# Kernel tuning notes

Measured on AMD Instinct MI355X. Metric: run time of the kernel, lower is better.

The kernel has to match this reference:

```python
import jax, jax.numpy as jnp
import numpy as np

N_NODES = 100000


def gcn_conv(x, src, dst, norm, W, b, n_nodes):
    # x: [N, Din]; src/dst: [E'] (with self-loops); norm: [E']
    h = x @ W  # [N, Dout] dense transform first (PyG GCNConv order)
    msgs = h[src] * norm[:, None]  # gather + degree scaling, [E', Dout]
    out = jax.ops.segment_sum(msgs, dst, num_segments=n_nodes)  # scatter-add
    return out + b


def setup_inputs() -> dict:
    key = jax.random.key(0)
    k_x, k_e, k_w1, k_w2 = jax.random.split(key, 4)
    input_dim, hidden_dim = 256, 128
    n_edges = 1600000
    x = jax.random.normal(k_x, (N_NODES, input_dim), dtype=jnp.float32)
    edge_index = jax.random.randint(k_e, (2, n_edges), 0, N_NODES, dtype=jnp.int64)
    # Glorot-style init for conv weights, zeros bias (PyG defaults)
    s1 = (6.0 / (input_dim + hidden_dim)) ** 0.5
    s2 = (6.0 / (hidden_dim + hidden_dim)) ** 0.5
    W1 = jax.random.uniform(k_w1, (input_dim, hidden_dim), jnp.float32, -s1, s1)
    W2 = jax.random.uniform(k_w2, (hidden_dim, hidden_dim), jnp.float32, -s2, s2)
    b1 = jnp.zeros((hidden_dim,), jnp.float32)
    b2 = jnp.zeros((hidden_dim,), jnp.float32)
    return {"x": x, "edge_index": edge_index, "W1": W1, "b1": b1, "W2": W2, "b2": b2}


def reference(x, edge_index, W1, b1, W2, b2):
    n = x.shape[0]
    loops = jnp.arange(n, dtype=edge_index.dtype)
    src = jnp.concatenate([edge_index[0], loops])  # add self-loops
    dst = jnp.concatenate([edge_index[1], loops])
    # symmetric normalization deg^-1/2 (in-degree including self-loops)
    deg = jax.ops.segment_sum(jnp.ones_like(dst, dtype=x.dtype), dst, num_segments=n)
    dinv = jax.lax.rsqrt(deg)
    norm = dinv[src] * dinv[dst]
    # layer 1: GCNConv -> ReLU (dropout is identity in eval mode)
    h = jax.nn.relu(gcn_conv(x, src, dst, norm, W1, b1, n))
    # layer 2
    h = jax.nn.relu(gcn_conv(h, src, dst, norm, W2, b2, n))
    return h
```

## Files before the change

kernel.cpp:

```cpp
#include <hip/hip_runtime.h>
#include <hip/hip_bf16.h>


#define DIN 256
#define DH 128
#define BKT_SHIFT 9
#define BKT_SZ 512
#define NBKT_MAX 256
#define CAP 10240

typedef __attribute__((ext_vector_type(8))) short short8;
typedef __attribute__((ext_vector_type(4))) float f32x4;
typedef __attribute__((ext_vector_type(2))) unsigned int uint2e;

__device__ __forceinline__ unsigned short f2bf(float f) {
    union { float f; unsigned int i; } c;
    c.f = f;
    unsigned int r = c.i + 0x7FFFu + ((c.i >> 16) & 1u);
    return (unsigned short)(r >> 16);
}
__device__ __forceinline__ float bf_lo(unsigned int u) {
    union { unsigned int i; float f; } c;
    c.i = u << 16;
    return c.f;
}
__device__ __forceinline__ float bf_hi(unsigned int u) {
    union { unsigned int i; float f; } c;
    c.i = u & 0xFFFF0000u;
    return c.f;
}

__global__ __launch_bounds__(256) void prep_k(const int* __restrict__ src,
                                              const int* __restrict__ dst,
                                              int* __restrict__ bcnt,
                                              int* __restrict__ tmp, int e, int n,
                                              int NBB,
                                              const float* __restrict__ W1,
                                              const float* __restrict__ W2,
                                              unsigned short* __restrict__ Wt1,
                                              unsigned short* __restrict__ Wt2) {
    int bx = blockIdx.x;
    int t = threadIdx.x;
    if (bx >= NBB) {
        int i = (bx - NBB) * 256 + t;
        if (i < 256 * 128) {
            int k = i >> 7, nn = i & 127;
            Wt1[(size_t)nn * 256 + k] = f2bf(W1[i]);
        } else if (i < 256 * 128 + 128 * 128) {
            int j = i - 256 * 128;
            int k = j >> 7, nn = j & 127;
            Wt2[(size_t)nn * 128 + k] = f2bf(W2[j]);
        }
        return;
    }
    __shared__ int hist[NBKT_MAX];
    __shared__ int rstart[NBKT_MAX];
    int nbkt = (n + BKT_SZ - 1) >> BKT_SHIFT;
    int chunk = (e + NBB - 1) / NBB;
    int beg = bx * chunk, end = min(e, beg + chunk);

    hist[t] = 0;
    __syncthreads();
    for (int i = beg + t; i < end; i += 256) atomicAdd(&hist[dst[i] >> BKT_SHIFT], 1);
    __syncthreads();
    int h = hist[t];
    if (t < nbkt && h > 0) rstart[t] = atomicAdd(&bcnt[t], h);
    __syncthreads();
    hist[t] = 0;
    __syncthreads();
    for (int i = beg + t; i < end; i += 256) {
        int d = dst[i];
        int b = d >> BKT_SHIFT;
        int o = atomicAdd(&hist[b], 1);
        tmp[(size_t)b * CAP + rstart[b] + o] = src[i] | ((d & (BKT_SZ - 1)) << 20);
    }
}

__global__ void scan196_k(const int* __restrict__ bcnt, int* __restrict__ base,
                          int* __restrict__ rowptr, int nbkt, int n) {
    __shared__ int s[256];
    int t = threadIdx.x;
    s[t] = (t < nbkt) ? bcnt[t] : 0;
    __syncthreads();
    for (int off = 1; off < 256; off <<= 1) {
        int x = (t >= off) ? s[t - off] : 0;
        __syncthreads();
        s[t] += x;
        __syncthreads();
    }
    base[t] = (t == 0) ? 0 : s[t - 1];
    if (t == nbkt - 1) {
        base[nbkt] = s[t];
        rowptr[n] = s[t];
    }
}

__global__ __launch_bounds__(1024) void scatter2_k(const int* __restrict__ tmp,
                                                   const int* __restrict__ bcnt,
                                                   const int* __restrict__ base,
                                                   float* __restrict__ dinv,
                                                   int* __restrict__ rowptr,
                                                   int* __restrict__ einfo, int n) {
    __shared__ int hist[BKT_SZ];
    __shared__ int scn[BKT_SZ];
    __shared__ int cur[BKT_SZ];
    int b = blockIdx.x;
    int t = threadIdx.x;
    int lo = b << BKT_SHIFT;
    int nn = min(n - lo, BKT_SZ);
    int cnt = bcnt[b];
    int bas = base[b];
    const int* rec = tmp + (size_t)b * CAP;
    if (t < BKT_SZ) hist[t] = 0;
    __syncthreads();
    for (int i = t; i < cnt; i += 1024) atomicAdd(&hist[(rec[i] >> 20) & (BKT_SZ - 1)], 1);
    __syncthreads();
    if (t < BKT_SZ) scn[t] = hist[t];
    __syncthreads();
    for (int off = 1; off < BKT_SZ; off <<= 1) {
        int x = 0;
        if (t < BKT_SZ && t >= off) x = scn[t - off];
        __syncthreads();
        if (t < BKT_SZ) scn[t] += x;
        __syncthreads();
    }
    if (t < nn) {
        int excl = bas + scn[t] - hist[t];
        dinv[lo + t] = 1.0f / sqrtf((float)(hist[t] + 1));
        rowptr[lo + t] = excl;
        cur[t] = excl;
    }
    __syncthreads();
    for (int i = t; i < cnt; i += 1024) {
        int r = rec[i];
        int dlow = (r >> 20) & (BKT_SZ - 1);
        int pos = atomicAdd(&cur[dlow], 1);
        einfo[pos] = r & 0xFFFFF;
    }
}

template <bool A_BF16>
__global__ __launch_bounds__(256) void gemm_mfma(const void* __restrict__ Av,
                                                 const unsigned short* __restrict__ Wt,
                                                 const float* __restrict__ dinv,
                                                 unsigned short* __restrict__ Hb,
                                                 int M, int K) {
    __shared__ unsigned short Bt[16384];
    const int t = threadIdx.x;
    const int w = t >> 6;
    const int lane = t & 63;
    const int l15 = lane & 15;
    const int quad = lane >> 4;
    const int row0 = blockIdx.x * 128 + w * 32;

    const float* Af = (const float*)Av;
    const unsigned short* Ab = (const unsigned short*)Av;

    f32x4 acc[2][8];
#pragma unroll
    for (int rt = 0; rt < 2; ++rt)
#pragma unroll
        for (int ct = 0; ct < 8; ++ct)
#pragma unroll
            for (int j = 0; j < 4; ++j) acc[rt][ct][j] = 0.0f;

    for (int kc = 0; kc < K; kc += 128) {
        if (kc) __syncthreads();
#pragma unroll
        for (int i = 0; i < 8; ++i) {
            int fg = w * 8 + i;
            int ks = fg >> 3, ct = fg & 7;
            int nn = ct * 16 + l15;
            int gk = ks * 32 + quad * 8;
            *(short8*)&Bt[fg * 512 + lane * 8] =
                *(const short8*)(Wt + (size_t)nn * K + kc + gk);
        }
        __syncthreads();
#pragma unroll
        for (int ks = 0; ks < 4; ++ks) {
            int kk = ks * 32 + quad * 8;
            short8 af[2];
#pragma unroll
            for (int rt = 0; rt < 2; ++rt) {
                int row = row0 + rt * 16 + l15;
                if (row < M) {
                    if (A_BF16) {
                        af[rt] = *(const short8*)(Ab + (size_t)row * K + kc + kk);
                    } else {
                        const float* p = Af + (size_t)row * K + kc + kk;
                        float4 x0 = *(const float4*)p;
                        float4 x1 = *(const float4*)(p + 4);
                        af[rt][0] = (short)f2bf(x0.x);
                        af[rt][1] = (short)f2bf(x0.y);
                        af[rt][2] = (short)f2bf(x0.z);
                        af[rt][3] = (short)f2bf(x0.w);
                        af[rt][4] = (short)f2bf(x1.x);
                        af[rt][5] = (short)f2bf(x1.y);
                        af[rt][6] = (short)f2bf(x1.z);
                        af[rt][7] = (short)f2bf(x1.w);
                    }
                } else {
#pragma unroll
                    for (int j = 0; j < 8; ++j) af[rt][j] = 0;
                }
            }
#pragma unroll
            for (int ct = 0; ct < 8; ++ct) {
                short8 bfr = *(const short8*)&Bt[(ks * 8 + ct) * 512 + lane * 8];
                acc[0][ct] = __builtin_amdgcn_mfma_f32_16x16x32_bf16(af[0], bfr, acc[0][ct], 0, 0, 0);
                acc[1][ct] = __builtin_amdgcn_mfma_f32_16x16x32_bf16(af[1], bfr, acc[1][ct], 0, 0, 0);
            }
        }
    }
#pragma unroll
    for (int rt = 0; rt < 2; ++rt)
#pragma unroll
        for (int r = 0; r < 4; ++r) {
            int row = row0 + rt * 16 + quad * 4 + r;
            if (row < M) {
                float dv = dinv[row];
                unsigned short* o = Hb + (size_t)row * 128 + l15;
#pragma unroll
                for (int ct = 0; ct < 8; ++ct) o[ct * 16] = f2bf(dv * acc[rt][ct][r]);
            }
        }
}

template <bool OUT_BF16>
__global__ __launch_bounds__(256) void agg_k(const unsigned short* __restrict__ Hb,
                                             const int* __restrict__ rowptr,
                                             const int* __restrict__ einfo,
                                             const float* __restrict__ dinv,
                                             const float* __restrict__ bias,
                                             void* __restrict__ out, int n) {
    int v = blockIdx.x * 4 + (threadIdx.x >> 6);
    int lane = threadIdx.x & 63;
    if (v >= n) return;
    int l = lane & 31, half = lane >> 5;
    const uint2* __restrict__ H = (const uint2*)Hb;
    float a0 = 0.f, a1 = 0.f, a2 = 0.f, a3 = 0.f;
    if (half == 0) {
        uint2 hv = H[(size_t)v * 32 + l];
        a0 = bf_lo(hv.x); a1 = bf_hi(hv.x);
        a2 = bf_lo(hv.y); a3 = bf_hi(hv.y);
    }
    int end = rowptr[v + 1];
    int i = rowptr[v] + half;
    for (; i + 6 < end; i += 8) {
        int s0 = __builtin_nontemporal_load(&einfo[i]);
        int s1 = __builtin_nontemporal_load(&einfo[i + 2]);
        int s2 = __builtin_nontemporal_load(&einfo[i + 4]);
        int s3 = __builtin_nontemporal_load(&einfo[i + 6]);
        uint2 v0 = H[(size_t)s0 * 32 + l];
        uint2 v1 = H[(size_t)s1 * 32 + l];
        uint2 v2 = H[(size_t)s2 * 32 + l];
        uint2 v3 = H[(size_t)s3 * 32 + l];
        a0 += bf_lo(v0.x); a1 += bf_hi(v0.x); a2 += bf_lo(v0.y); a3 += bf_hi(v0.y);
        a0 += bf_lo(v1.x); a1 += bf_hi(v1.x); a2 += bf_lo(v1.y); a3 += bf_hi(v1.y);
        a0 += bf_lo(v2.x); a1 += bf_hi(v2.x); a2 += bf_lo(v2.y); a3 += bf_hi(v2.y);
        a0 += bf_lo(v3.x); a1 += bf_hi(v3.x); a2 += bf_lo(v3.y); a3 += bf_hi(v3.y);
    }
    for (; i < end; i += 2) {
        int s = __builtin_nontemporal_load(&einfo[i]);
        uint2 vv = H[(size_t)s * 32 + l];
        a0 += bf_lo(vv.x); a1 += bf_hi(vv.x); a2 += bf_lo(vv.y); a3 += bf_hi(vv.y);
    }
    a0 += __shfl_xor(a0, 32);
    a1 += __shfl_xor(a1, 32);
    a2 += __shfl_xor(a2, 32);
    a3 += __shfl_xor(a3, 32);
    if (half == 0) {
        float dv = dinv[v];
        float4 bb = ((const float4*)bias)[l];
        float o0 = fmaxf(fmaf(dv, a0, bb.x), 0.f);
        float o1 = fmaxf(fmaf(dv, a1, bb.y), 0.f);
        float o2 = fmaxf(fmaf(dv, a2, bb.z), 0.f);
        float o3 = fmaxf(fmaf(dv, a3, bb.w), 0.f);
        if (OUT_BF16) {
            uint2e p;
            p.x = (unsigned int)f2bf(o0) | ((unsigned int)f2bf(o1) << 16);
            p.y = (unsigned int)f2bf(o2) | ((unsigned int)f2bf(o3) << 16);
            __builtin_nontemporal_store(p, (uint2e*)out + (size_t)v * 32 + l);
        } else {
            f32x4 o = {o0, o1, o2, o3};
            __builtin_nontemporal_store(o, (f32x4*)out + (size_t)v * 32 + l);
        }
    }
}

static inline size_t align_up(size_t x, size_t a) { return (x + a - 1) & ~(a - 1); }

extern "C" void kernel_launch(void* const* d_in, const int* in_sizes, int n_in,
                              void* d_out, int out_size, void* d_ws, size_t ws_size,
                              hipStream_t stream) {
    const float* x  = (const float*)d_in[0];
    const int*   ei = (const int*)d_in[1];
    const float* W1 = (const float*)d_in[2];
    const float* b1 = (const float*)d_in[3];
    const float* W2 = (const float*)d_in[4];
    const float* b2 = (const float*)d_in[5];

    const int N = in_sizes[0] / DIN;
    const int E = in_sizes[1] / 2;
    const int* src = ei;
    const int* dst = ei + E;
    const int NBKT = (N + BKT_SZ - 1) >> BKT_SHIFT;

    char* base_p = (char*)d_ws;
    size_t off = 0;
    int* bcnt = (int*)(base_p + off);       off = align_up(off + 256 * 4, 256);
    int* bbase = (int*)(base_p + off);      off = align_up(off + 257 * 4, 256);
    int* rowptr = (int*)(base_p + off);     off = align_up(off + (size_t)(N + 1) * 4, 256);
    float* dinv = (float*)(base_p + off);   off = align_up(off + (size_t)N * 4, 256);
    int* tmp = (int*)(base_p + off);        off = align_up(off + (size_t)NBKT * CAP * 4, 256);
    int* einfo = (int*)(base_p + off);      off = align_up(off + (size_t)E * 4, 256);
    unsigned short* Wt1 = (unsigned short*)(base_p + off); off = align_up(off + (size_t)128 * 256 * 2, 256);
    unsigned short* Wt2 = (unsigned short*)(base_p + off); off = align_up(off + (size_t)128 * 128 * 2, 256);
    unsigned short* hb  = (unsigned short*)(base_p + off); off = align_up(off + (size_t)N * 128 * 2, 256);
    unsigned short* a1b = (unsigned short*)(base_p + off); off = align_up(off + (size_t)N * 128 * 2, 256);

    float* out = (float*)d_out;

    const int NBB = 512;
    const int WTB = (256 * 128 + 128 * 128 + 255) / 256;

    hipMemsetAsync(bcnt, 0, 256 * sizeof(int), stream);
    prep_k<<<NBB + WTB, 256, 0, stream>>>(src, dst, bcnt, tmp, E, N, NBB, W1, W2, Wt1, Wt2);
    scan196_k<<<1, 256, 0, stream>>>(bcnt, bbase, rowptr, NBKT, N);
    scatter2_k<<<NBKT, 1024, 0, stream>>>(tmp, bcnt, bbase, dinv, rowptr, einfo, N);

    const int GB = (N + 127) / 128;
    gemm_mfma<false><<<GB, 256, 0, stream>>>(x, Wt1, dinv, hb, N, DIN);
    agg_k<true><<<(N + 3) / 4, 256, 0, stream>>>(hb, rowptr, einfo, dinv, b1, a1b, N);
    gemm_mfma<true><<<GB, 256, 0, stream>>>(a1b, Wt2, dinv, hb, N, DH);
    agg_k<false><<<(N + 3) / 4, 256, 0, stream>>>(hb, rowptr, einfo, dinv, b2, out, N);
}
```

Before: 429.3 us.

## Fuse edge bucketing with layer-1 GEMM and fold scan into scatter

Layer 1's GEMM no longer depends on dinv. It now runs in the same launch as the edge-bucketing blocks, and the source-side degree scaling moves into the first aggregation as a per-edge dinv gather. The single-block bucket scan is folded into scatter2_k, where each block redoes the 256-entry scan. The memset is replaced by a zeroing block in the weight-convert kernel. Together this cuts launches and serial dependencies at the cost of an extra random dinv load per edge in layer-1 aggregation.

```diff
diff --git a/kernel.cpp b/kernel.cpp
--- a/kernel.cpp
+++ b/kernel.cpp
@@ -30,128 +30,41 @@
     return c.f;
 }
 
-__global__ __launch_bounds__(256) void prep_k(const int* __restrict__ src,
-                                              const int* __restrict__ dst,
-                                              int* __restrict__ bcnt,
-                                              int* __restrict__ tmp, int e, int n,
-                                              int NBB,
-                                              const float* __restrict__ W1,
-                                              const float* __restrict__ W2,
-                                              unsigned short* __restrict__ Wt1,
-                                              unsigned short* __restrict__ Wt2) {
+__global__ __launch_bounds__(256) void cvt_zero_k(const float* __restrict__ W1,
+                                                  const float* __restrict__ W2,
+                                                  unsigned short* __restrict__ Wt1,
+                                                  unsigned short* __restrict__ Wt2,
+                                                  int* __restrict__ bcnt, int WTB) {
     int bx = blockIdx.x;
     int t = threadIdx.x;
-    if (bx >= NBB) {
-        int i = (bx - NBB) * 256 + t;
-        if (i < 256 * 128) {
-            int k = i >> 7, nn = i & 127;
-            Wt1[(size_t)nn * 256 + k] = f2bf(W1[i]);
-        } else if (i < 256 * 128 + 128 * 128) {
-            int j = i - 256 * 128;
-            int k = j >> 7, nn = j & 127;
-            Wt2[(size_t)nn * 128 + k] = f2bf(W2[j]);
-        }
+    if (bx >= WTB) {
+        bcnt[t] = 0;
         return;
     }
-    __shared__ int hist[NBKT_MAX];
-    __shared__ int rstart[NBKT_MAX];
-    int nbkt = (n + BKT_SZ - 1) >> BKT_SHIFT;
-    int chunk = (e + NBB - 1) / NBB;
-    int beg = bx * chunk, end = min(e, beg + chunk);
-
-    hist[t] = 0;
-    __syncthreads();
-    for (int i = beg + t; i < end; i += 256) atomicAdd(&hist[dst[i] >> BKT_SHIFT], 1);
-    __syncthreads();
-    int h = hist[t];
-    if (t < nbkt && h > 0) rstart[t] = atomicAdd(&bcnt[t], h);
-    __syncthreads();
-    hist[t] = 0;
-    __syncthreads();
-    for (int i = beg + t; i < end; i += 256) {
-        int d = dst[i];
-        int b = d >> BKT_SHIFT;
-        int o = atomicAdd(&hist[b], 1);
-        tmp[(size_t)b * CAP + rstart[b] + o] = src[i] | ((d & (BKT_SZ - 1)) << 20);
-    }
-}
-
-__global__ void scan196_k(const int* __restrict__ bcnt, int* __restrict__ base,
-                          int* __restrict__ rowptr, int nbkt, int n) {
-    __shared__ int s[256];
-    int t = threadIdx.x;
-    s[t] = (t < nbkt) ? bcnt[t] : 0;
-    __syncthreads();
-    for (int off = 1; off < 256; off <<= 1) {
-        int x = (t >= off) ? s[t - off] : 0;
-        __syncthreads();
-        s[t] += x;
-        __syncthreads();
-    }
-    base[t] = (t == 0) ? 0 : s[t - 1];
-    if (t == nbkt - 1) {
-        base[nbkt] = s[t];
-        rowptr[n] = s[t];
-    }
-}
-
-__global__ __launch_bounds__(1024) void scatter2_k(const int* __restrict__ tmp,
-                                                   const int* __restrict__ bcnt,
-                                                   const int* __restrict__ base,
-                                                   float* __restrict__ dinv,
-                                                   int* __restrict__ rowptr,
-                                                   int* __restrict__ einfo, int n) {
-    __shared__ int hist[BKT_SZ];
-    __shared__ int scn[BKT_SZ];
-    __shared__ int cur[BKT_SZ];
-    int b = blockIdx.x;
-    int t = threadIdx.x;
-    int lo = b << BKT_SHIFT;
-    int nn = min(n - lo, BKT_SZ);
-    int cnt = bcnt[b];
-    int bas = base[b];
-    const int* rec = tmp + (size_t)b * CAP;
-    if (t < BKT_SZ) hist[t] = 0;
-    __syncthreads();
-    for (int i = t; i < cnt; i += 1024) atomicAdd(&hist[(rec[i] >> 20) & (BKT_SZ - 1)], 1);
-    __syncthreads();
-    if (t < BKT_SZ) scn[t] = hist[t];
-    __syncthreads();
-    for (int off = 1; off < BKT_SZ; off <<= 1) {
-        int x = 0;
-        if (t < BKT_SZ && t >= off) x = scn[t - off];
-        __syncthreads();
-        if (t < BKT_SZ) scn[t] += x;
-        __syncthreads();
-    }
-    if (t < nn) {
-        int excl = bas + scn[t] - hist[t];
-        dinv[lo + t] = 1.0f / sqrtf((float)(hist[t] + 1));
-        rowptr[lo + t] = excl;
-        cur[t] = excl;
-    }
-    __syncthreads();
-    for (int i = t; i < cnt; i += 1024) {
-        int r = rec[i];
-        int dlow = (r >> 20) & (BKT_SZ - 1);
-        int pos = atomicAdd(&cur[dlow], 1);
-        einfo[pos] = r & 0xFFFFF;
-    }
-}
-
-template <bool A_BF16>
-__global__ __launch_bounds__(256) void gemm_mfma(const void* __restrict__ Av,
-                                                 const unsigned short* __restrict__ Wt,
-                                                 const float* __restrict__ dinv,
-                                                 unsigned short* __restrict__ Hb,
-                                                 int M, int K) {
-    __shared__ unsigned short Bt[16384];
+    int i = bx * 256 + t;
+    if (i < 256 * 128) {
+        int k = i >> 7, nn = i & 127;
+        Wt1[(size_t)nn * 256 + k] = f2bf(W1[i]);
+    } else {
+        int j = i - 256 * 128;
+        int k = j >> 7, nn = j & 127;
+        Wt2[(size_t)nn * 128 + k] = f2bf(W2[j]);
+    }
+}
+
+template <bool A_BF16, bool SCALE>
+__device__ __forceinline__ void gemm_body(unsigned short* Bt, int gb,
+                                          const void* __restrict__ Av,
+                                          const unsigned short* __restrict__ Wt,
+                                          const float* __restrict__ dinv,
+                                          unsigned short* __restrict__ Hb,
+                                          int M, int K) {
     const int t = threadIdx.x;
     const int w = t >> 6;
     const int lane = t & 63;
     const int l15 = lane & 15;
     const int quad = lane >> 4;
-    const int row0 = blockIdx.x * 128 + w * 32;
+    const int row0 = gb * 128 + w * 32;
 
     const float* Af = (const float*)Av;
     const unsigned short* Ab = (const unsigned short*)Av;
@@ -218,15 +131,121 @@
         for (int r = 0; r < 4; ++r) {
             int row = row0 + rt * 16 + quad * 4 + r;
             if (row < M) {
-                float dv = dinv[row];
+                float dv = SCALE ? dinv[row] : 1.0f;
                 unsigned short* o = Hb + (size_t)row * 128 + l15;
 #pragma unroll
-                for (int ct = 0; ct < 8; ++ct) o[ct * 16] = f2bf(dv * acc[rt][ct][r]);
+                for (int ct = 0; ct < 8; ++ct)
+                    o[ct * 16] = f2bf(SCALE ? dv * acc[rt][ct][r] : acc[rt][ct][r]);
             }
         }
 }
 
-template <bool OUT_BF16>
+struct SmemFused {
+    union {
+        unsigned short Bt[16384];
+        struct {
+            int hist[NBKT_MAX];
+            int rstart[NBKT_MAX];
+        } bk;
+    };
+};
+
+__global__ __launch_bounds__(256) void fused1_k(const int* __restrict__ src,
+                                                const int* __restrict__ dst,
+                                                int* __restrict__ bcnt,
+                                                int* __restrict__ tmp, int e, int n,
+                                                int NBB,
+                                                const float* __restrict__ x,
+                                                const unsigned short* __restrict__ Wt1,
+                                                unsigned short* __restrict__ hb, int M) {
+    __shared__ SmemFused sm;
+    int bx = blockIdx.x;
+    int t = threadIdx.x;
+    if (bx < NBB) {
+        int* hist = sm.bk.hist;
+        int* rstart = sm.bk.rstart;
+        int chunk = (e + NBB - 1) / NBB;
+        int beg = bx * chunk, end = min(e, beg + chunk);
+
+        hist[t] = 0;
+        __syncthreads();
+        for (int i = beg + t; i < end; i += 256) atomicAdd(&hist[dst[i] >> BKT_SHIFT], 1);
+        __syncthreads();
+        int nbkt = (n + BKT_SZ - 1) >> BKT_SHIFT;
+        int h = hist[t];
+        if (t < nbkt && h > 0) rstart[t] = atomicAdd(&bcnt[t], h);
+        __syncthreads();
+        hist[t] = 0;
+        __syncthreads();
+        for (int i = beg + t; i < end; i += 256) {
+            int d = dst[i];
+            int b = d >> BKT_SHIFT;
+            int o = atomicAdd(&hist[b], 1);
+            tmp[(size_t)b * CAP + rstart[b] + o] = src[i] | ((d & (BKT_SZ - 1)) << 20);
+        }
+        return;
+    }
+    gemm_body<false, false>(sm.Bt, bx - NBB, x, Wt1, nullptr, hb, M, DIN);
+}
+
+__global__ __launch_bounds__(1024) void scatter2_k(const int* __restrict__ tmp,
+                                                   const int* __restrict__ bcnt,
+                                                   float* __restrict__ dinv,
+                                                   int* __restrict__ rowptr,
+                                                   int* __restrict__ einfo, int n,
+                                                   int nbkt) {
+    __shared__ int hist[BKT_SZ];
+    __shared__ int scn[BKT_SZ];
+    __shared__ int cur[BKT_SZ];
+    int b = blockIdx.x;
+    int t = threadIdx.x;
+    int lo = b << BKT_SHIFT;
+    int nn = min(n - lo, BKT_SZ);
+    int cnt = bcnt[b];
+    const int* rec = tmp + (size_t)b * CAP;
+
+    if (t < 256) scn[t] = (t < nbkt) ? bcnt[t] : 0;
+    __syncthreads();
+    for (int off = 1; off < 256; off <<= 1) {
+        int v = 0;
+        if (t < 256 && t >= off) v = scn[t - off];
+        __syncthreads();
+        if (t < 256) scn[t] += v;
+        __syncthreads();
+    }
+    int bas = scn[b] - cnt;
+    if (b == nbkt - 1 && t == 0) rowptr[n] = scn[nbkt - 1];
+    __syncthreads();
+
+    if (t < BKT_SZ) hist[t] = 0;
+    __syncthreads();
+    for (int i = t; i < cnt; i += 1024) atomicAdd(&hist[(rec[i] >> 20) & (BKT_SZ - 1)], 1);
+    __syncthreads();
+    if (t < BKT_SZ) scn[t] = hist[t];
+    __syncthreads();
+    for (int off = 1; off < BKT_SZ; off <<= 1) {
+        int v = 0;
+        if (t < BKT_SZ && t >= off) v = scn[t - off];
+        __syncthreads();
+        if (t < BKT_SZ) scn[t] += v;
+        __syncthreads();
+    }
+    if (t < nn) {
+        int excl = bas + scn[t] - hist[t];
+        dinv[lo + t] = 1.0f / sqrtf((float)(hist[t] + 1));
+        rowptr[lo + t] = excl;
+        cur[t] = excl;
+    }
+    __syncthreads();
+    for (int i = t; i < cnt; i += 1024) {
+        int r = rec[i];
+        int dlow = (r >> 20) & (BKT_SZ - 1);
+        int pos = atomicAdd(&cur[dlow], 1);
+        einfo[pos] = r & 0xFFFFF;
+    }
+}
+
+template <bool SCALE_SRC, bool OUT_BF16>
 __global__ __launch_bounds__(256) void agg_k(const unsigned short* __restrict__ Hb,
                                              const int* __restrict__ rowptr,
                                              const int* __restrict__ einfo,
@@ -238,11 +257,17 @@
     if (v >= n) return;
     int l = lane & 31, half = lane >> 5;
     const uint2* __restrict__ H = (const uint2*)Hb;
+    float dv = dinv[v];
     float a0 = 0.f, a1 = 0.f, a2 = 0.f, a3 = 0.f;
     if (half == 0) {
         uint2 hv = H[(size_t)v * 32 + l];
-        a0 = bf_lo(hv.x); a1 = bf_hi(hv.x);
-        a2 = bf_lo(hv.y); a3 = bf_hi(hv.y);
+        if (SCALE_SRC) {
+            a0 = dv * bf_lo(hv.x); a1 = dv * bf_hi(hv.x);
+            a2 = dv * bf_lo(hv.y); a3 = dv * bf_hi(hv.y);
+        } else {
+            a0 = bf_lo(hv.x); a1 = bf_hi(hv.x);
+            a2 = bf_lo(hv.y); a3 = bf_hi(hv.y);
+        }
     }
     int end = rowptr[v + 1];
     int i = rowptr[v] + half;
@@ -251,26 +276,44 @@
         int s1 = __builtin_nontemporal_load(&einfo[i + 2]);
         int s2 = __builtin_nontemporal_load(&einfo[i + 4]);
         int s3 = __builtin_nontemporal_load(&einfo[i + 6]);
+        float d0 = 1.f, d1 = 1.f, d2 = 1.f, d3 = 1.f;
+        if (SCALE_SRC) { d0 = dinv[s0]; d1 = dinv[s1]; d2 = dinv[s2]; d3 = dinv[s3]; }
         uint2 v0 = H[(size_t)s0 * 32 + l];
         uint2 v1 = H[(size_t)s1 * 32 + l];
         uint2 v2 = H[(size_t)s2 * 32 + l];
         uint2 v3 = H[(size_t)s3 * 32 + l];
-        a0 += bf_lo(v0.x); a1 += bf_hi(v0.x); a2 += bf_lo(v0.y); a3 += bf_hi(v0.y);
-        a0 += bf_lo(v1.x); a1 += bf_hi(v1.x); a2 += bf_lo(v1.y); a3 += bf_hi(v1.y);
-        a0 += bf_lo(v2.x); a1 += bf_hi(v2.x); a2 += bf_lo(v2.y); a3 += bf_hi(v2.y);
-        a0 += bf_lo(v3.x); a1 += bf_hi(v3.x); a2 += bf_lo(v3.y); a3 += bf_hi(v3.y);
+        if (SCALE_SRC) {
+            a0 = fmaf(d0, bf_lo(v0.x), a0); a1 = fmaf(d0, bf_hi(v0.x), a1);
+            a2 = fmaf(d0, bf_lo(v0.y), a2); a3 = fmaf(d0, bf_hi(v0.y), a3);
+            a0 = fmaf(d1, bf_lo(v1.x), a0); a1 = fmaf(d1, bf_hi(v1.x), a1);
+            a2 = fmaf(d1, bf_lo(v1.y), a2); a3 = fmaf(d1, bf_hi(v1.y), a3);
+            a0 = fmaf(d2, bf_lo(v2.x), a0); a1 = fmaf(d2, bf_hi(v2.x), a1);
+            a2 = fmaf(d2, bf_lo(v2.y), a2); a3 = fmaf(d2, bf_hi(v2.y), a3);
+            a0 = fmaf(d3, bf_lo(v3.x), a0); a1 = fmaf(d3, bf_hi(v3.x), a1);
+            a2 = fmaf(d3, bf_lo(v3.y), a2); a3 = fmaf(d3, bf_hi(v3.y), a3);
+        } else {
+            a0 += bf_lo(v0.x); a1 += bf_hi(v0.x); a2 += bf_lo(v0.y); a3 += bf_hi(v0.y);
+            a0 += bf_lo(v1.x); a1 += bf_hi(v1.x); a2 += bf_lo(v1.y); a3 += bf_hi(v1.y);
+            a0 += bf_lo(v2.x); a1 += bf_hi(v2.x); a2 += bf_lo(v2.y); a3 += bf_hi(v2.y);
+            a0 += bf_lo(v3.x); a1 += bf_hi(v3.x); a2 += bf_lo(v3.y); a3 += bf_hi(v3.y);
+        }
     }
     for (; i < end; i += 2) {
         int s = __builtin_nontemporal_load(&einfo[i]);
+        float ds = SCALE_SRC ? dinv[s] : 1.f;
         uint2 vv = H[(size_t)s * 32 + l];
-        a0 += bf_lo(vv.x); a1 += bf_hi(vv.x); a2 += bf_lo(vv.y); a3 += bf_hi(vv.y);
+        if (SCALE_SRC) {
+            a0 = fmaf(ds, bf_lo(vv.x), a0); a1 = fmaf(ds, bf_hi(vv.x), a1);
+            a2 = fmaf(ds, bf_lo(vv.y), a2); a3 = fmaf(ds, bf_hi(vv.y), a3);
+        } else {
+            a0 += bf_lo(vv.x); a1 += bf_hi(vv.x); a2 += bf_lo(vv.y); a3 += bf_hi(vv.y);
+        }
     }
     a0 += __shfl_xor(a0, 32);
     a1 += __shfl_xor(a1, 32);
     a2 += __shfl_xor(a2, 32);
     a3 += __shfl_xor(a3, 32);
     if (half == 0) {
-        float dv = dinv[v];
         float4 bb = ((const float4*)bias)[l];
         float o0 = fmaxf(fmaf(dv, a0, bb.x), 0.f);
         float o1 = fmaxf(fmaf(dv, a1, bb.y), 0.f);
@@ -288,6 +331,15 @@
     }
 }
 
+__global__ __launch_bounds__(256) void gemm2_k(const unsigned short* __restrict__ A,
+                                               const unsigned short* __restrict__ Wt,
+                                               const float* __restrict__ dinv,
+                                               unsigned short* __restrict__ Hb,
+                                               int M, int K) {
+    __shared__ unsigned short Bt[16384];
+    gemm_body<true, true>(Bt, blockIdx.x, A, Wt, dinv, Hb, M, K);
+}
+
 static inline size_t align_up(size_t x, size_t a) { return (x + a - 1) & ~(a - 1); }
 
 extern "C" void kernel_launch(void* const* d_in, const int* in_sizes, int n_in,
@@ -309,7 +361,6 @@
     char* base_p = (char*)d_ws;
     size_t off = 0;
     int* bcnt = (int*)(base_p + off);       off = align_up(off + 256 * 4, 256);
-    int* bbase = (int*)(base_p + off);      off = align_up(off + 257 * 4, 256);
     int* rowptr = (int*)(base_p + off);     off = align_up(off + (size_t)(N + 1) * 4, 256);
     float* dinv = (float*)(base_p + off);   off = align_up(off + (size_t)N * 4, 256);
     int* tmp = (int*)(base_p + off);        off = align_up(off + (size_t)NBKT * CAP * 4, 256);
@@ -323,15 +374,12 @@
 
     const int NBB = 512;
     const int WTB = (256 * 128 + 128 * 128 + 255) / 256;
-
-    hipMemsetAsync(bcnt, 0, 256 * sizeof(int), stream);
-    prep_k<<<NBB + WTB, 256, 0, stream>>>(src, dst, bcnt, tmp, E, N, NBB, W1, W2, Wt1, Wt2);
-    scan196_k<<<1, 256, 0, stream>>>(bcnt, bbase, rowptr, NBKT, N);
-    scatter2_k<<<NBKT, 1024, 0, stream>>>(tmp, bcnt, bbase, dinv, rowptr, einfo, N);
-
     const int GB = (N + 127) / 128;
-    gemm_mfma<false><<<GB, 256, 0, stream>>>(x, Wt1, dinv, hb, N, DIN);
-    agg_k<true><<<(N + 3) / 4, 256, 0, stream>>>(hb, rowptr, einfo, dinv, b1, a1b, N);
-    gemm_mfma<true><<<GB, 256, 0, stream>>>(a1b, Wt2, dinv, hb, N, DH);
-    agg_k<false><<<(N + 3) / 4, 256, 0, stream>>>(hb, rowptr, einfo, dinv, b2, out, N);
-}
+
+    cvt_zero_k<<<WTB + 1, 256, 0, stream>>>(W1, W2, Wt1, Wt2, bcnt, WTB);
+    fused1_k<<<NBB + GB, 256, 0, stream>>>(src, dst, bcnt, tmp, E, N, NBB, x, Wt1, hb, N);
+    scatter2_k<<<NBKT, 1024, 0, stream>>>(tmp, bcnt, dinv, rowptr, einfo, N, NBKT);
+    agg_k<true, true><<<(N + 3) / 4, 256, 0, stream>>>(hb, rowptr, einfo, dinv, b1, a1b, N);
+    gemm2_k<<<GB, 256, 0, stream>>>(a1b, Wt2, dinv, hb, N, DH);
+    agg_k<false, false><<<(N + 3) / 4, 256, 0, stream>>>(hb, rowptr, einfo, dinv, b2, out, N);
+}
```

After: 410.8 us. 4.3% less time.
